# Performance work log

Measured on AMD Instinct MI355X. Metric: run time of the kernel, lower is better.

## Reference

```python
import jax, jax.numpy as jnp
import numpy as np

B, S, D, E, T = 16, 128, 128, 64, 128  # batch, seq_len, token_dim, dep_dim, transformed_dim (T==D required by mask broadcast)
V_TOK, V_DEP = 100000, 64
DEPTH = 2


def setup_inputs() -> dict:
    key = jax.random.key(0)
    ks = jax.random.split(key, 12)
    return {
        "token_table": jax.random.normal(ks[0], (V_TOK, D), jnp.float32) * 0.1,
        "dep_table": jax.random.normal(ks[1], (V_DEP, E), jnp.float32) * 0.1,
        # Bilinear(D, E, T): weight [T, D, E], bias [T]
        "W1": jax.random.normal(ks[2], (T, D, E), jnp.float32) * 0.05,
        "b1": jax.random.normal(ks[3], (T,), jnp.float32) * 0.05,
        # Bilinear(D, T, D): weight [D, D, T], bias [D]
        "W2": jax.random.normal(ks[4], (D, D, T), jnp.float32) * 0.05,
        "b2": jax.random.normal(ks[5], (D,), jnp.float32) * 0.05,
        # Linear(S, 1): weight [S] (flattened [1,S]), bias [1]
        "wr": jax.random.normal(ks[6], (S,), jnp.float32) * 0.05,
        "br": jax.random.normal(ks[7], (1,), jnp.float32) * 0.05,
        "tokens": jax.random.randint(ks[8], (B, S), 0, V_TOK),
        "dep_types": jax.random.randint(ks[9], (B, S), 0, V_DEP),
        "dep_heads": jax.random.randint(ks[10], (B, S), 0, S),
    }


def _block(tok, dep_emb, heads, W1, b1, W2, b2, wr, br):
    # tok: [B,S,D], dep_emb: [B,S,E], heads: [B,S] with values in [0,S)
    b, s, d = tok.shape
    # dep_transform (Bilinear) + mask + tanh. Masked structure: full tensor
    # tde_full[b,i,j,:] = tde[b,j,:] if heads[b,j]==i else 0 (heads<S always here),
    # and tanh(0)=0, so only the i==heads[b,j] rows are nonzero after activation.
    tde = jnp.tanh(jnp.einsum('bsd,tde,bse->bst', tok, W1, dep_emb) + b1)  # [B,S,T]
    # composition bilinear at the nonzero (i==head) positions
    c_nz = jnp.tanh(jnp.einsum('bsd,pdt,bst->bsp', tok, W2, tde) + b2)    # [B,S,D]
    # at masked positions tde_full==0 -> composition output is tanh(bias)
    c_bg = jnp.tanh(b2)                                                   # [D]
    # reduction Linear(S,1): out[b,i,:] = sum_j wr[j]*c[b,i,j,:] + br
    base = jnp.sum(wr) * c_bg + br                                        # [D]
    delta = wr[None, :, None] * (c_nz - c_bg)                             # [B,S,D]
    seg = (jnp.arange(b)[:, None] * s + heads).reshape(-1)                # scatter target i=heads[b,j]
    scat = jax.ops.segment_sum(delta.reshape(b * s, d), seg, num_segments=b * s)
    return base + scat.reshape(b, s, d)


def reference(token_table, dep_table, W1, b1, W2, b2, wr, br, tokens, dep_types, dep_heads):
    tok = token_table[tokens]          # [B,S,D]
    dep = dep_table[dep_types]         # [B,S,E]
    for _ in range(DEPTH):
        tok = _block(tok, dep, dep_heads, W1, b1, W2, b2, wr, br)
    out_mask = (dep_heads == 0)[..., None].astype(tok.dtype)  # keep only root tokens
    return tok * out_mask
```

## Files before the change

kernel.cpp:

```cpp
#include <hip/hip_runtime.h>
#include <hip/hip_bf16.h>

#define BB 16
#define SS 128
#define DD 128
#define EE 64
#define TT 128
#define NN (BB*SS)
#define KSPLIT 16

typedef __attribute__((ext_vector_type(8))) short short8;
typedef __attribute__((ext_vector_type(4))) float f32x4;
typedef __attribute__((ext_vector_type(4))) unsigned int u32x4;

__device__ inline unsigned pkbf16(float a, float b) {
    unsigned r;
    asm volatile("v_cvt_pk_bf16_f32 %0, %1, %2" : "=v"(r) : "v"(a), "v"(b));
    return r;
}
__device__ inline float bflo(unsigned u) { return __builtin_bit_cast(float, (unsigned)(u << 16)); }
__device__ inline float bfhi(unsigned u) { return __builtin_bit_cast(float, (unsigned)(u & 0xffff0000u)); }

__global__ __launch_bounds__(256) void k_prep(const float* __restrict__ W1,
                                              const float* __restrict__ dep_table,
                                              const float* __restrict__ W2,
                                              const float* __restrict__ token_table,
                                              const int* __restrict__ tokens,
                                              const float* __restrict__ b2,
                                              const float* __restrict__ wr,
                                              const float* __restrict__ br,
                                              __hip_bfloat16* __restrict__ G1,
                                              __hip_bfloat16* __restrict__ W2b,
                                              float* __restrict__ tok,
                                              float* __restrict__ basics) {
    int bid = blockIdx.x;
    int tid = threadIdx.x;
    if (bid < 256) {
        int bx = bid & 63, by = bid >> 6;
        int td = bx * 256 + tid;
        int v0 = by * 16;
        const float* w1row = W1 + (size_t)td * 64;
        float acc[16] = {};
#pragma unroll
        for (int e0 = 0; e0 < 64; e0 += 8) {
            f32x4 wa = *(const f32x4*)(w1row + e0);
            f32x4 wb = *(const f32x4*)(w1row + e0 + 4);
#pragma unroll
            for (int v = 0; v < 16; v++) {
                const float* dr = dep_table + (v0 + v) * 64 + e0;
                acc[v] += wa[0] * dr[0] + wa[1] * dr[1] + wa[2] * dr[2] + wa[3] * dr[3]
                        + wb[0] * dr[4] + wb[1] * dr[5] + wb[2] * dr[6] + wb[3] * dr[7];
            }
        }
#pragma unroll
        for (int v = 0; v < 16; v++)
            G1[(size_t)(v0 + v) * (TT * DD) + td] = __float2bfloat16(acc[v]);
    } else if (bid < 1280) {
        int cid = (bid - 256) * 256 + tid;
        int d = cid >> 11;
        int rem = cid & 2047;
        int p = rem >> 4;
        int sp = rem & 15;
        int h = sp >> 3, s = sp & 7;
        int t0 = h * 64 + ((s ^ (p & 7))) * 8;
        const float* src = W2 + ((size_t)p * 128 + d) * 128 + t0;
        f32x4 a = *(const f32x4*)(src);
        f32x4 b = *(const f32x4*)(src + 4);
        u32x4 o;
        o[0] = pkbf16(a[0], a[1]);
        o[1] = pkbf16(a[2], a[3]);
        o[2] = pkbf16(b[0], b[1]);
        o[3] = pkbf16(b[2], b[3]);
        *(u32x4*)((char*)W2b + (size_t)cid * 16) = o;
    } else if (bid < 2304) {
        int gid = (bid - 1280) * 256 + tid;
        int n = gid >> 7, dcol = gid & 127;
        tok[gid] = token_table[(size_t)tokens[n] * 128 + dcol];
    } else {
        __shared__ float red[128];
        int t = tid;
        if (t < 128) red[t] = wr[t];
        __syncthreads();
        for (int s = 64; s > 0; s >>= 1) {
            if (t < s) red[t] += red[t + s];
            __syncthreads();
        }
        if (t < 128) {
            float swr = red[0];
            float cbg = tanhf(b2[t]);
            basics[t] = cbg;
            basics[128 + t] = swr * cbg + br[0];
        }
    }
}

__global__ void k_tde(const float* __restrict__ tok, const int* __restrict__ dep_types,
                      const float* __restrict__ b1, const __hip_bfloat16* __restrict__ G1,
                      float* __restrict__ tde) {
    int n = blockIdx.x;
    int t = threadIdx.x;
    int v = dep_types[n];
    const float* trow = tok + (size_t)n * 128;
    const unsigned* g = (const unsigned*)(G1 + (size_t)v * (TT * DD) + t * 128);
    float acc = b1[t];
#pragma unroll
    for (int i = 0; i < 16; i++) {
        u32x4 w = *(const u32x4*)(g + i * 4);
        acc += trow[i * 8 + 0] * bflo(w[0]) + trow[i * 8 + 1] * bfhi(w[0]);
        acc += trow[i * 8 + 2] * bflo(w[1]) + trow[i * 8 + 3] * bfhi(w[1]);
        acc += trow[i * 8 + 4] * bflo(w[2]) + trow[i * 8 + 5] * bfhi(w[2]);
        acc += trow[i * 8 + 6] * bflo(w[3]) + trow[i * 8 + 7] * bfhi(w[3]);
    }
    tde[(size_t)n * 128 + t] = tanhf(acc);
}

#define LDS_SWZ(row, bcol) ((row) * 256 + ((bcol) ^ (((row) & 7) << 4)))

__global__ __launch_bounds__(256) void k_gemm(const float* __restrict__ tok,
                                              const float* __restrict__ tde,
                                              const __hip_bfloat16* __restrict__ W2b,
                                              float* __restrict__ part) {
    __shared__ char As[16384];
    __shared__ char Bs[32768];
    int nb = blockIdx.x, ks = blockIdx.y;
    int tid = threadIdx.x;
    int lane = tid & 63, w = tid >> 6;
    int wm = w >> 1, wp = w & 1;
    int n0 = nb * 64, d0 = ks * 8;
    int lrow = lane & 15, lk = lane >> 4;
    int r = tid >> 2, q = tid & 3;

    f32x4 acc[2][4] = {};

    for (int dd = 0; dd < 8; dd++) {
        int d = d0 + dd;
        const char* bsrc = (const char*)W2b + (size_t)d * 32768;
#pragma unroll
        for (int i = 0; i < 8; i++) {
            int off = (i * 256 + tid) * 16;
            *(u32x4*)(Bs + off) = *(const u32x4*)(bsrc + off);
        }
        float tokv = tok[(size_t)(n0 + r) * 128 + d];
        const float* trow = tde + (size_t)(n0 + r) * 128 + q * 32;
#pragma unroll
        for (int s = 0; s < 4; s++) {
            f32x4 x = *(const f32x4*)(trow + s * 8);
            f32x4 y = *(const f32x4*)(trow + s * 8 + 4);
            u32x4 val;
            val[0] = pkbf16(x[0] * tokv, x[1] * tokv);
            val[1] = pkbf16(x[2] * tokv, x[3] * tokv);
            val[2] = pkbf16(y[0] * tokv, y[1] * tokv);
            val[3] = pkbf16(y[2] * tokv, y[3] * tokv);
            int bcol = q * 64 + s * 16;
            *(u32x4*)(As + LDS_SWZ(r, bcol)) = val;
        }
        __syncthreads();
#pragma unroll
        for (int kk = 0; kk < 4; kk++) {
            short8 aF[2], bF[4];
#pragma unroll
            for (int mi = 0; mi < 2; mi++) {
                int row = wm * 32 + mi * 16 + lrow;
                aF[mi] = *(const short8*)(As + LDS_SWZ(row, kk * 64 + lk * 16));
            }
#pragma unroll
            for (int pj = 0; pj < 4; pj++) {
                int row = wp * 64 + pj * 16 + lrow;
                bF[pj] = *(const short8*)(Bs + LDS_SWZ(row, kk * 64 + lk * 16));
            }
#pragma unroll
            for (int mi = 0; mi < 2; mi++)
#pragma unroll
                for (int pj = 0; pj < 4; pj++)
                    acc[mi][pj] = __builtin_amdgcn_mfma_f32_16x16x32_bf16(
                        aF[mi], bF[pj], acc[mi][pj], 0, 0, 0);
        }
        __syncthreads();
    }
    float* pout = part + (size_t)ks * NN * 128;
#pragma unroll
    for (int mi = 0; mi < 2; mi++)
#pragma unroll
        for (int pj = 0; pj < 4; pj++)
#pragma unroll
            for (int rr = 0; rr < 4; rr++) {
                int row = wm * 32 + mi * 16 + (lane >> 4) * 4 + rr;
                int col = wp * 64 + pj * 16 + (lane & 15);
                pout[(size_t)(n0 + row) * 128 + col] = acc[mi][pj][rr];
            }
}

__global__ void k_e1(const float* __restrict__ part, const float* __restrict__ b2,
                     const float* __restrict__ wr, const float* __restrict__ basics,
                     float* __restrict__ delta) {
    int gid = blockIdx.x * 256 + threadIdx.x;
    int p = gid & 127;
    int n = gid >> 7;
    float s = 0.f;
#pragma unroll
    for (int k = 0; k < KSPLIT; k++) s += part[(size_t)k * NN * 128 + gid];
    float c = tanhf(s + b2[p]);
    delta[gid] = wr[n & 127] * (c - basics[p]);
}

__global__ void k_e2(const float* __restrict__ delta, const int* __restrict__ heads,
                     const float* __restrict__ basics, float* __restrict__ outp, int final_mask) {
    int bi = blockIdx.x;
    int b = bi >> 7, i = bi & 127;
    int p = threadIdx.x;
    __shared__ int hs[128];
    hs[p] = heads[b * 128 + p];
    __syncthreads();
    float acc = basics[128 + p];
    for (int j = 0; j < 128; j++) {
        if (hs[j] == i) acc += delta[(size_t)(b * 128 + j) * 128 + p];
    }
    if (final_mask) {
        outp[(size_t)bi * 128 + p] = (hs[i] == 0) ? acc : 0.f;
    } else {
        outp[(size_t)bi * 128 + p] = acc;
    }
}

extern "C" void kernel_launch(void* const* d_in, const int* in_sizes, int n_in,
                              void* d_out, int out_size, void* d_ws, size_t ws_size,
                              hipStream_t stream) {
    const float* token_table = (const float*)d_in[0];
    const float* dep_table   = (const float*)d_in[1];
    const float* W1          = (const float*)d_in[2];
    const float* b1          = (const float*)d_in[3];
    const float* W2          = (const float*)d_in[4];
    const float* b2          = (const float*)d_in[5];
    const float* wr          = (const float*)d_in[6];
    const float* br          = (const float*)d_in[7];
    const int* tokens        = (const int*)d_in[8];
    const int* dep_types     = (const int*)d_in[9];
    const int* dep_heads     = (const int*)d_in[10];
    float* out = (float*)d_out;

    char* ws = (char*)d_ws;
    __hip_bfloat16* G1  = (__hip_bfloat16*)(ws);
    __hip_bfloat16* W2b = (__hip_bfloat16*)(ws + (2ull << 20));
    float* tok    = (float*)(ws + (6ull << 20));
    float* tde    = (float*)(ws + (7ull << 20));
    float* delta  = (float*)(ws + (8ull << 20));
    float* part   = (float*)(ws + (9ull << 20));
    float* basics = (float*)(ws + (25ull << 20));

    k_prep<<<2305, 256, 0, stream>>>(W1, dep_table, W2, token_table, tokens,
                                     b2, wr, br, G1, W2b, tok, basics);

    for (int depth = 0; depth < 2; depth++) {
        k_tde<<<NN, 128, 0, stream>>>(tok, dep_types, b1, G1, tde);
        k_gemm<<<dim3(32, KSPLIT), 256, 0, stream>>>(tok, tde, W2b, part);
        k_e1<<<1024, 256, 0, stream>>>(part, b2, wr, basics, delta);
        k_e2<<<NN, 128, 0, stream>>>(delta, dep_heads, basics,
                                     (depth == 1) ? out : tok, depth == 1);
    }
}
```

Measured before the change: 119.0 us.

## Fuse split-K reduction epilogue into GEMM via last-block atomic tickets

Removes the separate k_e1 launch by having the last split-K block for each row tile, found through an atomic ticket counter, sum the partials and apply tanh and the delta scaling inside the GEMM kernel. Tickets are zeroed in the prep kernel. The G1 prep section is also shrunk from 256 blocks to 64 blocks that each loop over four vocabulary chunks. The aim is to save a launch and a pass over memory, but the reduction is serialized onto a single block per tile, and the G1 prep now has less parallelism.

```diff
diff --git a/kernel.cpp b/kernel.cpp
--- a/kernel.cpp
+++ b/kernel.cpp
@@ -20,6 +20,8 @@
 }
 __device__ inline float bflo(unsigned u) { return __builtin_bit_cast(float, (unsigned)(u << 16)); }
 __device__ inline float bfhi(unsigned u) { return __builtin_bit_cast(float, (unsigned)(u & 0xffff0000u)); }
+
+#define LDS_SWZ(row, bcol) ((row) * 256 + ((bcol) ^ (((row) & 7) << 4)))
 
 __global__ __launch_bounds__(256) void k_prep(const float* __restrict__ W1,
                                               const float* __restrict__ dep_table,
@@ -32,31 +34,32 @@
                                               __hip_bfloat16* __restrict__ G1,
                                               __hip_bfloat16* __restrict__ W2b,
                                               float* __restrict__ tok,
-                                              float* __restrict__ basics) {
+                                              float* __restrict__ basics,
+                                              unsigned* __restrict__ tickets) {
     int bid = blockIdx.x;
     int tid = threadIdx.x;
-    if (bid < 256) {
-        int bx = bid & 63, by = bid >> 6;
-        int td = bx * 256 + tid;
-        int v0 = by * 16;
+    if (bid < 64) {
+        int td = bid * 256 + tid;
         const float* w1row = W1 + (size_t)td * 64;
-        float acc[16] = {};
-#pragma unroll
-        for (int e0 = 0; e0 < 64; e0 += 8) {
-            f32x4 wa = *(const f32x4*)(w1row + e0);
-            f32x4 wb = *(const f32x4*)(w1row + e0 + 4);
-#pragma unroll
-            for (int v = 0; v < 16; v++) {
-                const float* dr = dep_table + (v0 + v) * 64 + e0;
-                acc[v] += wa[0] * dr[0] + wa[1] * dr[1] + wa[2] * dr[2] + wa[3] * dr[3]
-                        + wb[0] * dr[4] + wb[1] * dr[5] + wb[2] * dr[6] + wb[3] * dr[7];
-            }
-        }
-#pragma unroll
-        for (int v = 0; v < 16; v++)
-            G1[(size_t)(v0 + v) * (TT * DD) + td] = __float2bfloat16(acc[v]);
-    } else if (bid < 1280) {
-        int cid = (bid - 256) * 256 + tid;
+        for (int vc = 0; vc < 4; vc++) {
+            float acc[16] = {};
+#pragma unroll
+            for (int e0 = 0; e0 < 64; e0 += 8) {
+                f32x4 wa = *(const f32x4*)(w1row + e0);
+                f32x4 wb = *(const f32x4*)(w1row + e0 + 4);
+#pragma unroll
+                for (int v = 0; v < 16; v++) {
+                    const float* dr = dep_table + (vc * 16 + v) * 64 + e0;
+                    acc[v] += wa[0] * dr[0] + wa[1] * dr[1] + wa[2] * dr[2] + wa[3] * dr[3]
+                            + wb[0] * dr[4] + wb[1] * dr[5] + wb[2] * dr[6] + wb[3] * dr[7];
+                }
+            }
+#pragma unroll
+            for (int v = 0; v < 16; v++)
+                G1[(size_t)(vc * 16 + v) * (TT * DD) + td] = __float2bfloat16(acc[v]);
+        }
+    } else if (bid < 1088) {
+        int cid = (bid - 64) * 256 + tid;
         int d = cid >> 11;
         int rem = cid & 2047;
         int p = rem >> 4;
@@ -72,13 +75,14 @@
         o[2] = pkbf16(b[0], b[1]);
         o[3] = pkbf16(b[2], b[3]);
         *(u32x4*)((char*)W2b + (size_t)cid * 16) = o;
-    } else if (bid < 2304) {
-        int gid = (bid - 1280) * 256 + tid;
+    } else if (bid < 2112) {
+        int gid = (bid - 1088) * 256 + tid;
         int n = gid >> 7, dcol = gid & 127;
         tok[gid] = token_table[(size_t)tokens[n] * 128 + dcol];
     } else {
         __shared__ float red[128];
         int t = tid;
+        if (t < 64) tickets[t] = 0u;
         if (t < 128) red[t] = wr[t];
         __syncthreads();
         for (int s = 64; s > 0; s >>= 1) {
@@ -114,14 +118,19 @@
     tde[(size_t)n * 128 + t] = tanhf(acc);
 }
 
-#define LDS_SWZ(row, bcol) ((row) * 256 + ((bcol) ^ (((row) & 7) << 4)))
-
-__global__ __launch_bounds__(256) void k_gemm(const float* __restrict__ tok,
-                                              const float* __restrict__ tde,
-                                              const __hip_bfloat16* __restrict__ W2b,
-                                              float* __restrict__ part) {
+__global__ __launch_bounds__(256, 2) void k_gemmf(const float* __restrict__ tok,
+                                                  const float* __restrict__ tde,
+                                                  const __hip_bfloat16* __restrict__ W2b,
+                                                  float* __restrict__ part,
+                                                  float* __restrict__ delta,
+                                                  const float* __restrict__ basics,
+                                                  const float* __restrict__ wr,
+                                                  const float* __restrict__ b2,
+                                                  unsigned* __restrict__ tickets,
+                                                  int dep) {
     __shared__ char As[16384];
     __shared__ char Bs[32768];
+    __shared__ int last;
     int nb = blockIdx.x, ks = blockIdx.y;
     int tid = threadIdx.x;
     int lane = tid & 63, w = tid >> 6;
@@ -188,19 +197,27 @@
                 int col = wp * 64 + pj * 16 + (lane & 15);
                 pout[(size_t)(n0 + row) * 128 + col] = acc[mi][pj][rr];
             }
-}
-
-__global__ void k_e1(const float* __restrict__ part, const float* __restrict__ b2,
-                     const float* __restrict__ wr, const float* __restrict__ basics,
-                     float* __restrict__ delta) {
-    int gid = blockIdx.x * 256 + threadIdx.x;
-    int p = gid & 127;
-    int n = gid >> 7;
-    float s = 0.f;
-#pragma unroll
-    for (int k = 0; k < KSPLIT; k++) s += part[(size_t)k * NN * 128 + gid];
-    float c = tanhf(s + b2[p]);
-    delta[gid] = wr[n & 127] * (c - basics[p]);
+
+    __threadfence();
+    __syncthreads();
+    if (tid == 0) {
+        unsigned got = __hip_atomic_fetch_add(&tickets[dep * 32 + nb], 1u,
+                                              __ATOMIC_ACQ_REL, __HIP_MEMORY_SCOPE_AGENT);
+        last = (got == KSPLIT - 1);
+    }
+    __syncthreads();
+    if (last) {
+        for (int pass = 0; pass < 32; pass++) {
+            int g = pass * 256 + tid;
+            int row = g >> 7, p = g & 127;
+            int gg = (n0 + row) * 128 + p;
+            float s = 0.f;
+#pragma unroll
+            for (int k = 0; k < KSPLIT; k++) s += part[(size_t)k * NN * 128 + gg];
+            float c = tanhf(s + b2[p]);
+            delta[gg] = wr[(n0 + row) & 127] * (c - basics[p]);
+        }
+    }
 }
 
 __global__ void k_e2(const float* __restrict__ delta, const int* __restrict__ heads,
@@ -246,14 +263,15 @@
     float* delta  = (float*)(ws + (8ull << 20));
     float* part   = (float*)(ws + (9ull << 20));
     float* basics = (float*)(ws + (25ull << 20));
-
-    k_prep<<<2305, 256, 0, stream>>>(W1, dep_table, W2, token_table, tokens,
-                                     b2, wr, br, G1, W2b, tok, basics);
+    unsigned* tickets = (unsigned*)(ws + (25ull << 20) + 8192);
+
+    k_prep<<<2113, 256, 0, stream>>>(W1, dep_table, W2, token_table, tokens,
+                                     b2, wr, br, G1, W2b, tok, basics, tickets);
 
     for (int depth = 0; depth < 2; depth++) {
         k_tde<<<NN, 128, 0, stream>>>(tok, dep_types, b1, G1, tde);
-        k_gemm<<<dim3(32, KSPLIT), 256, 0, stream>>>(tok, tde, W2b, part);
-        k_e1<<<1024, 256, 0, stream>>>(part, b2, wr, basics, delta);
+        k_gemmf<<<dim3(32, KSPLIT), 256, 0, stream>>>(tok, tde, W2b, part, delta,
+                                                      basics, wr, b2, tickets, depth);
         k_e2<<<NN, 128, 0, stream>>>(delta, dep_heads, basics,
                                      (depth == 1) ? out : tok, depth == 1);
     }
```

Measured after the change: 377.3 us. 217% more time.
